# Kernel tuning notes

Hardware: AMD Instinct MI355X
Metric: run time of the kernel (lower is better)

## Reference

```python
import jax, jax.numpy as jnp
import numpy as np

VAR_NUM, IN_DIM, OUT_DIM = 3, 8, 32
N_PTS, M_PTS, K_LAST = 8192, 2048, 10
RADIUS = 0.0342
PROJ_HIDDEN = 64
N_DIM = 2
MLP_DIMS = [2 * N_DIM + OUT_DIM, 80, 80, OUT_DIM]  # [36, 80, 80, 32]


def _gelu(x):
    # torch F.gelu default = exact erf form
    return jax.nn.gelu(x, approximate=False)


def _radius_neighbors(data, queries, r):
    # CSR-style neighbor lists (indices grouped per query), chunked for memory
    idx_chunks = []
    counts = np.zeros(queries.shape[0], np.int64)
    r2 = r * r
    for s in range(0, queries.shape[0], 1024):
        q = queries[s:s + 1024]
        d2 = ((q[:, None, :] - data[None, :, :]) ** 2).sum(-1)
        mask = d2 <= r2
        _, cols = np.nonzero(mask)  # row-major -> grouped by query
        idx_chunks.append(cols.astype(np.int32))
        counts[s:s + q.shape[0]] = mask.sum(1)
    return np.concatenate(idx_chunks), counts.astype(np.int32)


def _knn(data, queries, k):
    out = np.zeros((queries.shape[0], k), np.int32)
    for s in range(0, queries.shape[0], 1024):
        q = queries[s:s + 1024]
        d2 = ((q[:, None, :] - data[None, :, :]) ** 2).sum(-1)
        out[s:s + q.shape[0]] = np.argpartition(d2, k, axis=1)[:, :k]
    return out.reshape(-1)


def _mlp_params(key, dims):
    Ws, bs = [], []
    for i in range(len(dims) - 1):
        key, k1 = jax.random.split(key)
        Ws.append(jax.random.normal(k1, (dims[i], dims[i + 1]), jnp.float32) / np.sqrt(dims[i]).astype(np.float32))
        bs.append(jnp.zeros((dims[i + 1],), jnp.float32))
    return Ws, bs


def setup_inputs():
    rng = np.random.default_rng(0)
    input_grid = rng.uniform(size=(N_PTS, N_DIM)).astype(np.float32)
    output_grid = rng.uniform(size=(M_PTS, N_DIM)).astype(np.float32)
    nbr_index, nbr_counts = _radius_neighbors(input_grid, input_grid, RADIUS)
    nbr_seg = np.repeat(np.arange(N_PTS, dtype=np.int32), nbr_counts)
    nbr_last_index = _knn(input_grid, output_grid, K_LAST)

    key = jax.random.key(0)
    ks = jax.random.split(key, 4)
    inp = jax.random.normal(ks[0], (1, N_PTS, VAR_NUM * IN_DIM), jnp.float32)
    pW, pb = _mlp_params(ks[1], [IN_DIM, PROJ_HIDDEN, OUT_DIM])
    it0_W, it0_b = _mlp_params(ks[2], MLP_DIMS)
    it1_W, it1_b = _mlp_params(ks[3], MLP_DIMS)
    return dict(
        inp=inp,
        input_grid=jnp.asarray(input_grid), output_grid=jnp.asarray(output_grid),
        proj_W0=pW[0], proj_b0=pb[0], proj_W1=pW[1], proj_b1=pb[1],
        it0_W0=it0_W[0], it0_b0=it0_b[0], it0_W1=it0_W[1], it0_b1=it0_b[1], it0_W2=it0_W[2], it0_b2=it0_b[2],
        it1_W0=it1_W[0], it1_b0=it1_b[0], it1_W1=it1_W[1], it1_b1=it1_b[1], it1_W2=it1_W[2], it1_b2=it1_b[2],
        nbr_index=jnp.asarray(nbr_index), nbr_seg=jnp.asarray(nbr_seg),
        nbr_counts=jnp.asarray(nbr_counts), nbr_last_index=jnp.asarray(nbr_last_index),
    )


def _mlp3(x, W0, b0, W1, b1, W2, b2):
    x = _gelu(x @ W0 + b0)
    x = _gelu(x @ W1 + b1)
    return x @ W2 + b2


def reference(inp, input_grid, output_grid, proj_W0, proj_b0, proj_W1, proj_b1,
              it0_W0, it0_b0, it0_W1, it0_b1, it0_W2, it0_b2,
              it1_W0, it1_b0, it1_W1, it1_b1, it1_W2, it1_b2,
              nbr_index, nbr_seg, nbr_counts, nbr_last_index):
    B, N, _ = inp.shape  # B must be 1 (module's IT indexing assumes it)
    x = inp.reshape(B * N, VAR_NUM, IN_DIM)
    # pointwise projection MLP (gelu between layers)
    x = _gelu(x @ proj_W0 + proj_b0) @ proj_W1 + proj_b1  # (N, V, OUT_DIM)

    inv_counts = (1.0 / jnp.maximum(nbr_counts, 1).astype(x.dtype))[:, None]
    y_pos = input_grid[nbr_index]        # (E, 2) neighbor positions
    self_pos = input_grid[nbr_seg]       # (E, 2) query positions
    last_y = input_grid[nbr_last_index]                    # (M*K, 2)
    last_self = jnp.repeat(output_grid, K_LAST, axis=0)    # (M*K, 2)

    outs = []
    for v in range(VAR_NUM):
        f = x[:, v, :]
        # IT layer 0: radius neighborhoods on input grid, residual add
        agg = jnp.concatenate([y_pos, self_pos, f[nbr_index]], axis=-1)  # (E, 36)
        h = _mlp3(agg, it0_W0, it0_b0, it0_W1, it0_b1, it0_W2, it0_b2)
        f = jax.ops.segment_sum(h, nbr_seg, num_segments=N) * inv_counts + f
        # IT layer 1 (last): fixed-K neighbors from input grid to output grid, mean
        agg = jnp.concatenate([last_y, last_self, f[nbr_last_index]], axis=-1)
        h = _mlp3(agg, it1_W0, it1_b0, it1_W1, it1_b1, it1_W2, it1_b2)
        outs.append(h.reshape(M_PTS, K_LAST, OUT_DIM).mean(axis=1))
    # original concatenates temp[None] along dim=2 -> (1, M, V*OUT_DIM)
    return jnp.concatenate(outs, axis=-1)[None]
```

## Files before the change

kernel.cpp:

```cpp
#include <hip/hip_runtime.h>
#include <hip/hip_bf16.h>
#include <math.h>

#define N_PTS 8192
#define M_PTS 2048
#define KLAST 10
#define VARS 3
#define OUTD 32
#define D1 80
#define D2 80
#define PB 4
#define LPTS 2
#define NT 256
#define NWAVES 4
#define NTL 256
#define NWL 4
#define RP 32

#define FRAG 512
#define W0F 10
#define W1F 15
#define W2F 6
#define WPACK ((W0F + W1F + W2F) * FRAG)

#define AKEYS (VARS * PB)
#define AKP   (AKEYS + 1)
#define LKEYS (LPTS * VARS)
#define LKP   (LKEYS + 1)

typedef float f4 __attribute__((ext_vector_type(4)));
typedef short bf16x8 __attribute__((ext_vector_type(8)));

__device__ __forceinline__ float gelu_f(float x) {
    float x2 = x * x;
    float s = x * __builtin_fmaf(0.1029418f, x2, 2.3022083f);
    float u = __builtin_amdgcn_exp2f(s);
    float r = __builtin_amdgcn_rcpf(u + 1.0f);
    return __builtin_fmaf(-x, r, x);
}
__device__ __forceinline__ unsigned short f2bf(float x) {
    unsigned int u = __float_as_uint(x);
    u += 0x7FFF + ((u >> 16) & 1);
    return (unsigned short)(u >> 16);
}
__device__ __forceinline__ float bf2f(unsigned short h) {
    return __uint_as_float(((unsigned int)h) << 16);
}
__device__ __forceinline__ int pk2(float a, float b) {
    __hip_bfloat162 h = __float22bfloat162_rn(float2{a, b});
    int r; __builtin_memcpy(&r, &h, 4); return r;
}
__device__ __forceinline__ bf16x8 mk8(int a, int b, int c, int d) {
    int4 v = make_int4(a, b, c, d);
    bf16x8 r; __builtin_memcpy(&r, &v, 16); return r;
}

__device__ __forceinline__ void pack_weights(
    const float* __restrict__ W0g, const float* __restrict__ W1g,
    const float* __restrict__ W2g, unsigned short* __restrict__ wp, int t)
{
    for (int idx = t; idx < W0F * FRAG; idx += 256) {
        int f = idx >> 9, r = idx & 511;
        int lane = r >> 3, e = r & 7;
        int lm = lane & 15, qd = lane >> 4;
        int cb = f >> 1, ks = f & 1;
        int col = cb * 16 + lm;
        int k = ks * 32 + qd * 8 + e;
        float w = (k < 32) ? W0g[(k + 4) * D1 + col]
                           : ((k < 36) ? W0g[(k - 32) * D1 + col] : 0.0f);
        wp[idx] = f2bf(w);
    }
    for (int idx = t; idx < W1F * FRAG; idx += 256) {
        int f = idx >> 9, r = idx & 511;
        int lane = r >> 3, e = r & 7;
        int lm = lane & 15, qd = lane >> 4;
        int cb = f / 3, ks = f - cb * 3;
        int col = cb * 16 + lm;
        int blk = 2 * ks + (e >> 2);
        int srow = blk * 16 + qd * 4 + (e & 3);
        wp[W0F * FRAG + idx] = f2bf((blk < 5) ? W1g[srow * D1 + col] : 0.0f);
    }
    for (int idx = t; idx < W2F * FRAG; idx += 256) {
        int f = idx >> 9, r = idx & 511;
        int lane = r >> 3, e = r & 7;
        int lm = lane & 15, qd = lane >> 4;
        int cb = f / 3, ks = f - cb * 3;
        int col = cb * 16 + lm;
        int blk = 2 * ks + (e >> 2);
        int srow = blk * 16 + qd * 4 + (e & 3);
        wp[(W0F + W1F) * FRAG + idx] = f2bf((blk < 5) ? W2g[srow * OUTD + col] : 0.0f);
    }
}

#define MFMA16(A, B, C) __builtin_amdgcn_mfma_f32_16x16x32_bf16(A, B, C, 0, 0, 0)
#define GPACK(ACC) make_int2(pk2(gelu_f(ACC.x), gelu_f(ACC.y)), \
                             pk2(gelu_f(ACC.z), gelu_f(ACC.w)))

__device__ __forceinline__ void mlp_chunk(
    int4 featsi, int2 posfi,
    const unsigned short* WA, const float* bs,
    int quad, int ckey, float* accH, int kp)
{
    bf16x8 b1f0; __builtin_memcpy(&b1f0, &featsi, 16);
    int4 pv = make_int4(posfi.x, posfi.y, 0, 0);
    bf16x8 b1f1; __builtin_memcpy(&b1f1, &pv, 16);

    int2 k0, k1, k2, k3, k4;
#define L1S(CB, PK) { \
    f4 acc = *(const f4*)&bs[(CB) * 16 + quad * 4]; \
    bf16x8 a0 = *(const bf16x8*)&WA[((CB) * 2 + 0) * FRAG]; \
    bf16x8 a1 = *(const bf16x8*)&WA[((CB) * 2 + 1) * FRAG]; \
    acc = MFMA16(a0, b1f0, acc); \
    acc = MFMA16(a1, b1f1, acc); \
    PK = GPACK(acc); }
    L1S(0, k0) L1S(1, k1) L1S(2, k2) L1S(3, k3) L1S(4, k4)
#undef L1S

    bf16x8 b20 = mk8(k0.x, k0.y, k1.x, k1.y);
    bf16x8 b21 = mk8(k2.x, k2.y, k3.x, k3.y);
    bf16x8 b22 = mk8(k4.x, k4.y, 0, 0);
    int2 q0, q1, q2, q3, q4;
#define L2S(CB, QK) { \
    f4 acc = *(const f4*)&bs[80 + (CB) * 16 + quad * 4]; \
    const unsigned short* wh = &WA[(W0F + (CB) * 3) * FRAG]; \
    bf16x8 h0 = *(const bf16x8*)&wh[0]; \
    bf16x8 h1 = *(const bf16x8*)&wh[FRAG]; \
    bf16x8 h2 = *(const bf16x8*)&wh[2 * FRAG]; \
    acc = MFMA16(h0, b20, acc); \
    acc = MFMA16(h1, b21, acc); \
    acc = MFMA16(h2, b22, acc); \
    QK = GPACK(acc); }
    L2S(0, q0) L2S(1, q1) L2S(2, q2) L2S(3, q3) L2S(4, q4)
#undef L2S

    bf16x8 b30 = mk8(q0.x, q0.y, q1.x, q1.y);
    bf16x8 b31 = mk8(q2.x, q2.y, q3.x, q3.y);
    bf16x8 b32 = mk8(q4.x, q4.y, 0, 0);
#define L3S(CB) { \
    f4 acc = *(const f4*)&bs[160 + (CB) * 16 + quad * 4]; \
    const unsigned short* wh = &WA[(W0F + W1F + (CB) * 3) * FRAG]; \
    bf16x8 h0 = *(const bf16x8*)&wh[0]; \
    bf16x8 h1 = *(const bf16x8*)&wh[FRAG]; \
    bf16x8 h2 = *(const bf16x8*)&wh[2 * FRAG]; \
    acc = MFMA16(h0, b30, acc); \
    acc = MFMA16(h1, b31, acc); \
    acc = MFMA16(h2, b32, acc); \
    if (ckey >= 0) { \
        float* ap = accH + ((CB) * 16 + quad * 4) * kp + ckey; \
        atomicAdd(&ap[0], acc.x); \
        atomicAdd(&ap[kp], acc.y); \
        atomicAdd(&ap[2 * kp], acc.z); \
        atomicAdd(&ap[3 * kp], acc.w); \
    } }
    L3S(0) L3S(1)
#undef L3S
}

__global__ __launch_bounds__(256) void proj_scan_kernel(
    const float* __restrict__ inp, const float* __restrict__ grid_in,
    const float* __restrict__ W0, const float* __restrict__ b0,
    const float* __restrict__ W1, const float* __restrict__ b1,
    unsigned short* __restrict__ f0b, int* __restrict__ posb,
    const int* __restrict__ counts, int* __restrict__ offsets,
    const float* __restrict__ i0W0, const float* __restrict__ i0W1,
    const float* __restrict__ i0W2, unsigned short* __restrict__ wpack0,
    const float* __restrict__ i1W0, const float* __restrict__ i1W1,
    const float* __restrict__ i1W2, unsigned short* __restrict__ wpack1)
{
    const int t = threadIdx.x;
    if (blockIdx.x == 769) { pack_weights(i0W0, i0W1, i0W2, wpack0, t); return; }
    if (blockIdx.x == 770) { pack_weights(i1W0, i1W1, i1W2, wpack1, t); return; }
    if (blockIdx.x == 768) {
        __shared__ int ws2[4], wx2[4];
        const int lane = t & 63, wave = t >> 6;
        int4 a[8];
#pragma unroll
        for (int i = 0; i < 8; ++i) a[i] = ((const int4*)counts)[t * 8 + i];
        int s = 0;
#pragma unroll
        for (int i = 0; i < 8; ++i) s += a[i].x + a[i].y + a[i].z + a[i].w;
        int x = s;
#pragma unroll
        for (int d = 1; d < 64; d <<= 1) {
            int y = __shfl_up(x, d);
            if (lane >= d) x += y;
        }
        if (lane == 63) ws2[wave] = x;
        __syncthreads();
        if (t == 0) {
            wx2[0] = 0;
            wx2[1] = ws2[0];
            wx2[2] = ws2[0] + ws2[1];
            wx2[3] = ws2[0] + ws2[1] + ws2[2];
        }
        __syncthreads();
        int base = wx2[wave] + (x - s);
#pragma unroll
        for (int i = 0; i < 8; ++i) {
            int4 c = a[i];
            int4 o;
            o.x = base; base += c.x;
            o.y = base; base += c.y;
            o.z = base; base += c.z;
            o.w = base; base += c.w;
            ((int4*)offsets)[t * 8 + i] = o;
        }
        return;
    }
    __shared__ float W0s[8 * 64];
    __shared__ float W1s[64 * OUTD];
    __shared__ float xs[32 * 8];
    __shared__ float H[32 * 64];
    const int r0 = blockIdx.x * 32;
    for (int idx = t; idx < 512; idx += 256) W0s[idx] = W0[idx];
    for (int idx = t; idx < 64 * OUTD; idx += 256) W1s[idx] = W1[idx];
    xs[t] = inp[r0 * 8 + t];
    if (t < 32) {
        int row = r0 + t, n = row / 3;
        posb[n] = pk2(grid_in[2 * n], grid_in[2 * n + 1]);
    }
    __syncthreads();
#pragma unroll 1
    for (int p = 0; p < 8; ++p) {
        int o = t + 256 * p, r = o >> 6, col = o & 63;
        float s = b0[col];
#pragma unroll
        for (int k = 0; k < 8; ++k) s += xs[r * 8 + k] * W0s[k * 64 + col];
        H[o] = gelu_f(s);
    }
    __syncthreads();
#pragma unroll 1
    for (int p = 0; p < 4; ++p) {
        int o = t + 256 * p, r = o >> 5, c = o & 31;
        float s = b1[c];
#pragma unroll 8
        for (int k = 0; k < 64; ++k) s += H[r * 64 + k] * W1s[k * OUTD + c];
        int row = r0 + r;
        int n = row / 3, v = row - n * 3;
        f0b[((size_t)(v << 13) + n) * RP + c] = f2bf(s);
    }
}

__global__ __launch_bounds__(256, 2) void agg_kernel(
    const float* __restrict__ grid_in, const unsigned short* __restrict__ f0b,
    const int* __restrict__ posb,
    const int* __restrict__ nbr_index, const int* __restrict__ offsets,
    const int* __restrict__ counts,
    const unsigned short* __restrict__ wpack,
    const float* __restrict__ b0g, const float* __restrict__ b1g,
    const float* __restrict__ b2g,
    unsigned short* __restrict__ f1b)
{
    __shared__ __attribute__((aligned(16))) unsigned short Wls[WPACK];
    __shared__ __attribute__((aligned(16))) float bs[192];
    __shared__ __attribute__((aligned(16))) float accH[OUTD * AKP];
    __shared__ int offs[PB + 1];
    __shared__ int px2b[PB];
    __shared__ float invb[PB];

    const int t = threadIdx.x;
    const int lane = t & 63;
    const int lm = lane & 15, quad = lane >> 4;
    const int wave = t >> 6;
    const int p0 = blockIdx.x * PB;

    for (int idx = t; idx < WPACK / 8; idx += NT)
        ((int4*)Wls)[idx] = ((const int4*)wpack)[idx];
    const unsigned short* WA = Wls + lane * 8;

    for (int idx = t; idx < 192; idx += NT)
        bs[idx] = (idx < 80) ? b0g[idx] : (idx < 160 ? b1g[idx - 80] : b2g[idx - 160]);
    if (t < PB) {
        offs[t] = offsets[p0 + t];
        int c = counts[p0 + t];
        invb[t] = 1.0f / (float)(c > 1 ? c : 1);
        px2b[t] = pk2(grid_in[2 * (p0 + t)], grid_in[2 * (p0 + t) + 1]);
    }
    if (t == PB) offs[PB] = offsets[p0 + PB - 1] + counts[p0 + PB - 1];
    for (int idx = t; idx < OUTD * AKP; idx += NT) accH[idx] = 0.0f;
    __syncthreads();

    const int e0 = offs[0];
    const int cntT = offs[PB] - e0;
    const int Rb = VARS * cntT;
    const int nch = (Rb + 15) >> 4;

    auto fetch_index = [&](int ch2, int& key, int& j) {
        key = -1; j = 0;
        if (ch2 < nch) {
            int myrow = (ch2 << 4) + lm;
            if (myrow < Rb) {
                int myv = (myrow >= 2 * cntT) ? 2 : ((myrow >= cntT) ? 1 : 0);
                int e = e0 + myrow - myv * cntT;
                int lp = 0;
#pragma unroll
                for (int l = 1; l < PB; ++l) lp += (e >= offs[l]);
                key = myv * PB + lp;
                j = nbr_index[e];
            }
        }
    };
    auto fetch_record = [&](int key, int j, int4& feats, int2& posf) {
        feats = make_int4(0, 0, 0, 0); posf = make_int2(0, 0);
        if (key >= 0) {
            int v = key >> 2, lp = key & 3;
            feats = ((const int4*)(f0b + ((size_t)(v << 13) + j) * RP))[quad];
            if (quad == 0) posf = make_int2(posb[j], px2b[lp]);
        }
    };

    int keyA, jA, keyB, jB;
    fetch_index(wave, keyA, jA);
    fetch_index(wave + NWAVES, keyB, jB);
    int4 featsA; int2 posfA;
    fetch_record(keyA, jA, featsA, posfA);

    for (int ch = wave; ch < nch; ch += NWAVES) {
        int ckey = keyA; int4 cf = featsA; int2 cp = posfA;
        keyA = keyB; jA = jB;
        fetch_index(ch + 2 * NWAVES, keyB, jB);
        fetch_record(keyA, jA, featsA, posfA);
        mlp_chunk(cf, cp, WA, bs, quad, ckey, accH, AKP);
    }
    __syncthreads();
    for (int idx = t; idx < VARS * PB * OUTD; idx += NT) {
        int key = idx >> 5, c = idx & 31;
        int v = key >> 2, lp = key & 3;
        size_t rec = ((size_t)(v << 13) + p0 + lp) * RP;
        float val = accH[c * AKP + key] * invb[lp] + bf2f(f0b[rec + c]);
        f1b[rec + c] = f2bf(val);
    }
}

__global__ __launch_bounds__(256, 2) void last_kernel(
    const unsigned short* __restrict__ f1b, const int* __restrict__ posb,
    const float* __restrict__ grid_out,
    const int* __restrict__ nbr_last,
    const unsigned short* __restrict__ wpack,
    const float* __restrict__ b0g, const float* __restrict__ b1g,
    const float* __restrict__ b2g,
    float* __restrict__ out)
{
    __shared__ __attribute__((aligned(16))) unsigned short Wls[WPACK];
    __shared__ __attribute__((aligned(16))) float bs[192];
    __shared__ __attribute__((aligned(16))) float accH[OUTD * LKP];
    __shared__ int pxo2b[LPTS];

    const int t = threadIdx.x;
    const int lane = t & 63;
    const int lm = lane & 15, quad = lane >> 4;
    const int wave = t >> 6;
    const int m0 = blockIdx.x * LPTS;

    for (int idx = t; idx < WPACK / 8; idx += NTL)
        ((int4*)Wls)[idx] = ((const int4*)wpack)[idx];
    const unsigned short* WA = Wls + lane * 8;

    for (int idx = t; idx < 192; idx += NTL)
        bs[idx] = (idx < 80) ? b0g[idx] : (idx < 160 ? b1g[idx - 80] : b2g[idx - 160]);
    if (t < LPTS)
        pxo2b[t] = pk2(grid_out[2 * (m0 + t)], grid_out[2 * (m0 + t) + 1]);
    for (int idx = t; idx < OUTD * LKP; idx += NTL) accH[idx] = 0.0f;
    __syncthreads();

    const int Rb = LPTS * VARS * KLAST;
    const int nch = (Rb + 15) >> 4;

    auto fetch_index = [&](int ch2, int& key, int& j) {
        key = -1; j = 0;
        if (ch2 < nch) {
            int myrow = (ch2 << 4) + lm;
            if (myrow < Rb) {
                int lp = myrow / 30, rr = myrow - lp * 30;
                int v = rr / KLAST, kk = rr - v * KLAST;
                j = nbr_last[(m0 + lp) * KLAST + kk];
                key = lp * VARS + v;
            }
        }
    };
    auto fetch_record = [&](int key, int j, int4& feats, int2& posf) {
        feats = make_int4(0, 0, 0, 0); posf = make_int2(0, 0);
        if (key >= 0) {
            int lp = key / VARS, v = key - lp * VARS;
            feats = ((const int4*)(f1b + ((size_t)(v << 13) + j) * RP))[quad];
            if (quad == 0) posf = make_int2(posb[j], pxo2b[lp]);
        }
    };

    int keyA, jA, keyB, jB;
    fetch_index(wave, keyA, jA);
    fetch_index(wave + NWL, keyB, jB);
    int4 featsA; int2 posfA;
    fetch_record(keyA, jA, featsA, posfA);

    for (int ch = wave; ch < nch; ch += NWL) {
        int ckey = keyA; int4 cf = featsA; int2 cp = posfA;
        keyA = keyB; jA = jB;
        fetch_index(ch + 2 * NWL, keyB, jB);
        fetch_record(keyA, jA, featsA, posfA);
        mlp_chunk(cf, cp, WA, bs, quad, ckey, accH, LKP);
    }
    __syncthreads();
    for (int idx = t; idx < LPTS * VARS * OUTD; idx += NTL) {
        int key = idx >> 5, c = idx & 31;
        int lp = key / VARS, v = key - lp * VARS;
        out[((size_t)(m0 + lp) * VARS + v) * OUTD + c] =
            accH[c * LKP + key] * (1.0f / KLAST);
    }
}

extern "C" void kernel_launch(void* const* d_in, const int* in_sizes, int n_in,
                              void* d_out, int out_size, void* d_ws, size_t ws_size,
                              hipStream_t stream) {
    const float* inp      = (const float*)d_in[0];
    const float* grid_in  = (const float*)d_in[1];
    const float* grid_out = (const float*)d_in[2];
    const float* pW0 = (const float*)d_in[3];
    const float* pb0 = (const float*)d_in[4];
    const float* pW1 = (const float*)d_in[5];
    const float* pb1 = (const float*)d_in[6];
    const float* i0W0 = (const float*)d_in[7];
    const float* i0b0 = (const float*)d_in[8];
    const float* i0W1 = (const float*)d_in[9];
    const float* i0b1 = (const float*)d_in[10];
    const float* i0W2 = (const float*)d_in[11];
    const float* i0b2 = (const float*)d_in[12];
    const float* i1W0 = (const float*)d_in[13];
    const float* i1b0 = (const float*)d_in[14];
    const float* i1W1 = (const float*)d_in[15];
    const float* i1b1 = (const float*)d_in[16];
    const float* i1W2 = (const float*)d_in[17];
    const float* i1b2 = (const float*)d_in[18];
    const int* nbr_index  = (const int*)d_in[19];
    const int* nbr_counts = (const int*)d_in[21];
    const int* nbr_last   = (const int*)d_in[22];

    unsigned short* f0b = (unsigned short*)d_ws;
    unsigned short* f1b = f0b + (size_t)VARS * N_PTS * RP;
    int* offsets = (int*)(f1b + (size_t)VARS * N_PTS * RP);
    int* posb    = offsets + N_PTS;
    unsigned short* wpack0 = (unsigned short*)(posb + N_PTS);
    unsigned short* wpack1 = wpack0 + WPACK;

    proj_scan_kernel<<<771, 256, 0, stream>>>(inp, grid_in, pW0, pb0, pW1, pb1,
                                              f0b, posb, nbr_counts, offsets,
                                              i0W0, i0W1, i0W2, wpack0,
                                              i1W0, i1W1, i1W2, wpack1);
    agg_kernel<<<N_PTS / PB, NT, 0, stream>>>(grid_in, f0b, posb, nbr_index, offsets,
                                              nbr_counts, wpack0,
                                              i0b0, i0b1, i0b2, f1b);
    last_kernel<<<M_PTS / LPTS, NTL, 0, stream>>>(f1b, posb, grid_out, nbr_last, wpack1,
                                                  i1b0, i1b1, i1b2,
                                                  (float*)d_out);
}
```

Before: 327.2 us.

## Process two neighbor chunks per wave with interleaved MFMA chains

The MLP chunk routine now handles two independent 16-row chunks at once, sharing the weight fragment loads and interleaving their MFMA accumulations to hide MFMA dependency latency. The aggregation loop issues prefetches for pairs of chunks, and the last-layer kernel doubles points per block (LPTS 4) so each wave processes exactly one pair with no loop. Launch bounds drop to one block per SIMD-pair to give room for the doubled register usage, which lowers occupancy.

```diff
diff --git a/kernel.cpp b/kernel.cpp
--- a/kernel.cpp
+++ b/kernel.cpp
@@ -10,7 +10,7 @@
 #define D1 80
 #define D2 80
 #define PB 4
-#define LPTS 2
+#define LPTS 4
 #define NT 256
 #define NWAVES 4
 #define NTL 256
@@ -96,61 +96,91 @@
 #define GPACK(ACC) make_int2(pk2(gelu_f(ACC.x), gelu_f(ACC.y)), \
                              pk2(gelu_f(ACC.z), gelu_f(ACC.w)))
 
-__device__ __forceinline__ void mlp_chunk(
-    int4 featsi, int2 posfi,
+__device__ __forceinline__ void mlp_chunk2(
+    int4 fAi, int2 pAi, int keyAc,
+    int4 fCi, int2 pCi, int keyCc,
     const unsigned short* WA, const float* bs,
-    int quad, int ckey, float* accH, int kp)
+    int quad, float* accH, int kp)
 {
-    bf16x8 b1f0; __builtin_memcpy(&b1f0, &featsi, 16);
-    int4 pv = make_int4(posfi.x, posfi.y, 0, 0);
-    bf16x8 b1f1; __builtin_memcpy(&b1f1, &pv, 16);
-
-    int2 k0, k1, k2, k3, k4;
-#define L1S(CB, PK) { \
-    f4 acc = *(const f4*)&bs[(CB) * 16 + quad * 4]; \
-    bf16x8 a0 = *(const bf16x8*)&WA[((CB) * 2 + 0) * FRAG]; \
-    bf16x8 a1 = *(const bf16x8*)&WA[((CB) * 2 + 1) * FRAG]; \
-    acc = MFMA16(a0, b1f0, acc); \
-    acc = MFMA16(a1, b1f1, acc); \
-    PK = GPACK(acc); }
-    L1S(0, k0) L1S(1, k1) L1S(2, k2) L1S(3, k3) L1S(4, k4)
+    bf16x8 a1f0; __builtin_memcpy(&a1f0, &fAi, 16);
+    int4 pva = make_int4(pAi.x, pAi.y, 0, 0);
+    bf16x8 a1f1; __builtin_memcpy(&a1f1, &pva, 16);
+    bf16x8 c1f0; __builtin_memcpy(&c1f0, &fCi, 16);
+    int4 pvc = make_int4(pCi.x, pCi.y, 0, 0);
+    bf16x8 c1f1; __builtin_memcpy(&c1f1, &pvc, 16);
+
+    int2 k0a, k1a, k2a, k3a, k4a, k0c, k1c, k2c, k3c, k4c;
+#define L1S(CB, PA, PC) { \
+    f4 bias = *(const f4*)&bs[(CB) * 16 + quad * 4]; \
+    bf16x8 w0 = *(const bf16x8*)&WA[((CB) * 2 + 0) * FRAG]; \
+    bf16x8 w1 = *(const bf16x8*)&WA[((CB) * 2 + 1) * FRAG]; \
+    f4 accA = bias, accC = bias; \
+    accA = MFMA16(w0, a1f0, accA); \
+    accC = MFMA16(w0, c1f0, accC); \
+    accA = MFMA16(w1, a1f1, accA); \
+    accC = MFMA16(w1, c1f1, accC); \
+    PA = GPACK(accA); PC = GPACK(accC); }
+    L1S(0, k0a, k0c) L1S(1, k1a, k1c) L1S(2, k2a, k2c)
+    L1S(3, k3a, k3c) L1S(4, k4a, k4c)
 #undef L1S
 
-    bf16x8 b20 = mk8(k0.x, k0.y, k1.x, k1.y);
-    bf16x8 b21 = mk8(k2.x, k2.y, k3.x, k3.y);
-    bf16x8 b22 = mk8(k4.x, k4.y, 0, 0);
-    int2 q0, q1, q2, q3, q4;
-#define L2S(CB, QK) { \
-    f4 acc = *(const f4*)&bs[80 + (CB) * 16 + quad * 4]; \
+    bf16x8 a20 = mk8(k0a.x, k0a.y, k1a.x, k1a.y);
+    bf16x8 a21 = mk8(k2a.x, k2a.y, k3a.x, k3a.y);
+    bf16x8 a22 = mk8(k4a.x, k4a.y, 0, 0);
+    bf16x8 c20 = mk8(k0c.x, k0c.y, k1c.x, k1c.y);
+    bf16x8 c21 = mk8(k2c.x, k2c.y, k3c.x, k3c.y);
+    bf16x8 c22 = mk8(k4c.x, k4c.y, 0, 0);
+    int2 q0a, q1a, q2a, q3a, q4a, q0c, q1c, q2c, q3c, q4c;
+#define L2S(CB, QA, QC) { \
+    f4 bias = *(const f4*)&bs[80 + (CB) * 16 + quad * 4]; \
     const unsigned short* wh = &WA[(W0F + (CB) * 3) * FRAG]; \
     bf16x8 h0 = *(const bf16x8*)&wh[0]; \
     bf16x8 h1 = *(const bf16x8*)&wh[FRAG]; \
     bf16x8 h2 = *(const bf16x8*)&wh[2 * FRAG]; \
-    acc = MFMA16(h0, b20, acc); \
-    acc = MFMA16(h1, b21, acc); \
-    acc = MFMA16(h2, b22, acc); \
-    QK = GPACK(acc); }
-    L2S(0, q0) L2S(1, q1) L2S(2, q2) L2S(3, q3) L2S(4, q4)
+    f4 accA = bias, accC = bias; \
+    accA = MFMA16(h0, a20, accA); \
+    accC = MFMA16(h0, c20, accC); \
+    accA = MFMA16(h1, a21, accA); \
+    accC = MFMA16(h1, c21, accC); \
+    accA = MFMA16(h2, a22, accA); \
+    accC = MFMA16(h2, c22, accC); \
+    QA = GPACK(accA); QC = GPACK(accC); }
+    L2S(0, q0a, q0c) L2S(1, q1a, q1c) L2S(2, q2a, q2c)
+    L2S(3, q3a, q3c) L2S(4, q4a, q4c)
 #undef L2S
 
-    bf16x8 b30 = mk8(q0.x, q0.y, q1.x, q1.y);
-    bf16x8 b31 = mk8(q2.x, q2.y, q3.x, q3.y);
-    bf16x8 b32 = mk8(q4.x, q4.y, 0, 0);
+    bf16x8 a30 = mk8(q0a.x, q0a.y, q1a.x, q1a.y);
+    bf16x8 a31 = mk8(q2a.x, q2a.y, q3a.x, q3a.y);
+    bf16x8 a32 = mk8(q4a.x, q4a.y, 0, 0);
+    bf16x8 c30 = mk8(q0c.x, q0c.y, q1c.x, q1c.y);
+    bf16x8 c31 = mk8(q2c.x, q2c.y, q3c.x, q3c.y);
+    bf16x8 c32 = mk8(q4c.x, q4c.y, 0, 0);
 #define L3S(CB) { \
-    f4 acc = *(const f4*)&bs[160 + (CB) * 16 + quad * 4]; \
+    f4 bias = *(const f4*)&bs[160 + (CB) * 16 + quad * 4]; \
     const unsigned short* wh = &WA[(W0F + W1F + (CB) * 3) * FRAG]; \
     bf16x8 h0 = *(const bf16x8*)&wh[0]; \
     bf16x8 h1 = *(const bf16x8*)&wh[FRAG]; \
     bf16x8 h2 = *(const bf16x8*)&wh[2 * FRAG]; \
-    acc = MFMA16(h0, b30, acc); \
-    acc = MFMA16(h1, b31, acc); \
-    acc = MFMA16(h2, b32, acc); \
-    if (ckey >= 0) { \
-        float* ap = accH + ((CB) * 16 + quad * 4) * kp + ckey; \
-        atomicAdd(&ap[0], acc.x); \
-        atomicAdd(&ap[kp], acc.y); \
-        atomicAdd(&ap[2 * kp], acc.z); \
-        atomicAdd(&ap[3 * kp], acc.w); \
+    f4 accA = bias, accC = bias; \
+    accA = MFMA16(h0, a30, accA); \
+    accC = MFMA16(h0, c30, accC); \
+    accA = MFMA16(h1, a31, accA); \
+    accC = MFMA16(h1, c31, accC); \
+    accA = MFMA16(h2, a32, accA); \
+    accC = MFMA16(h2, c32, accC); \
+    if (keyAc >= 0) { \
+        float* ap = accH + ((CB) * 16 + quad * 4) * kp + keyAc; \
+        atomicAdd(&ap[0], accA.x); \
+        atomicAdd(&ap[kp], accA.y); \
+        atomicAdd(&ap[2 * kp], accA.z); \
+        atomicAdd(&ap[3 * kp], accA.w); \
+    } \
+    if (keyCc >= 0) { \
+        float* ap = accH + ((CB) * 16 + quad * 4) * kp + keyCc; \
+        atomicAdd(&ap[0], accC.x); \
+        atomicAdd(&ap[kp], accC.y); \
+        atomicAdd(&ap[2 * kp], accC.z); \
+        atomicAdd(&ap[3 * kp], accC.w); \
     } }
     L3S(0) L3S(1)
 #undef L3S
@@ -241,7 +271,7 @@
     }
 }
 
-__global__ __launch_bounds__(256, 2) void agg_kernel(
+__global__ __launch_bounds__(256, 1) void agg_kernel(
     const float* __restrict__ grid_in, const unsigned short* __restrict__ f0b,
     const int* __restrict__ posb,
     const int* __restrict__ nbr_index, const int* __restrict__ offsets,
@@ -309,18 +339,24 @@
         }
     };
 
-    int keyA, jA, keyB, jB;
-    fetch_index(wave, keyA, jA);
-    fetch_index(wave + NWAVES, keyB, jB);
-    int4 featsA; int2 posfA;
-    fetch_record(keyA, jA, featsA, posfA);
-
-    for (int ch = wave; ch < nch; ch += NWAVES) {
-        int ckey = keyA; int4 cf = featsA; int2 cp = posfA;
-        keyA = keyB; jA = jB;
-        fetch_index(ch + 2 * NWAVES, keyB, jB);
-        fetch_record(keyA, jA, featsA, posfA);
-        mlp_chunk(cf, cp, WA, bs, quad, ckey, accH, AKP);
+    int keyA0, jA0, keyA1, jA1, keyB0, jB0, keyB1, jB1;
+    fetch_index(2 * wave, keyA0, jA0);
+    fetch_index(2 * wave + 1, keyA1, jA1);
+    fetch_index(2 * wave + 2 * NWAVES, keyB0, jB0);
+    fetch_index(2 * wave + 2 * NWAVES + 1, keyB1, jB1);
+    int4 fA0, fA1; int2 pA0, pA1;
+    fetch_record(keyA0, jA0, fA0, pA0);
+    fetch_record(keyA1, jA1, fA1, pA1);
+
+    for (int cc = 2 * wave; cc < nch; cc += 2 * NWAVES) {
+        int ck0 = keyA0, ck1 = keyA1;
+        int4 cf0 = fA0, cf1 = fA1; int2 cp0 = pA0, cp1 = pA1;
+        keyA0 = keyB0; jA0 = jB0; keyA1 = keyB1; jA1 = jB1;
+        fetch_index(cc + 4 * NWAVES, keyB0, jB0);
+        fetch_index(cc + 4 * NWAVES + 1, keyB1, jB1);
+        fetch_record(keyA0, jA0, fA0, pA0);
+        fetch_record(keyA1, jA1, fA1, pA1);
+        mlp_chunk2(cf0, cp0, ck0, cf1, cp1, ck1, WA, bs, quad, accH, AKP);
     }
     __syncthreads();
     for (int idx = t; idx < VARS * PB * OUTD; idx += NT) {
@@ -332,7 +368,7 @@
     }
 }
 
-__global__ __launch_bounds__(256, 2) void last_kernel(
+__global__ __launch_bounds__(256, 1) void last_kernel(
     const unsigned short* __restrict__ f1b, const int* __restrict__ posb,
     const float* __restrict__ grid_out,
     const int* __restrict__ nbr_last,
@@ -387,19 +423,14 @@
         }
     };
 
-    int keyA, jA, keyB, jB;
-    fetch_index(wave, keyA, jA);
-    fetch_index(wave + NWL, keyB, jB);
-    int4 featsA; int2 posfA;
-    fetch_record(keyA, jA, featsA, posfA);
-
-    for (int ch = wave; ch < nch; ch += NWL) {
-        int ckey = keyA; int4 cf = featsA; int2 cp = posfA;
-        keyA = keyB; jA = jB;
-        fetch_index(ch + 2 * NWL, keyB, jB);
-        fetch_record(keyA, jA, featsA, posfA);
-        mlp_chunk(cf, cp, WA, bs, quad, ckey, accH, LKP);
-    }
+    int keyA0, jA0, keyA1, jA1;
+    fetch_index(2 * wave, keyA0, jA0);
+    fetch_index(2 * wave + 1, keyA1, jA1);
+    int4 fA0, fA1; int2 pA0, pA1;
+    fetch_record(keyA0, jA0, fA0, pA0);
+    fetch_record(keyA1, jA1, fA1, pA1);
+    mlp_chunk2(fA0, pA0, keyA0, fA1, pA1, keyA1, WA, bs, quad, accH, LKP);
+
     __syncthreads();
     for (int idx = t; idx < LPTS * VARS * OUTD; idx += NTL) {
         int key = idx >> 5, c = idx & 31;
```

Measured after the change: 370.0 us. 1.13x slower.
